# Performance work log

Hardware: AMD Instinct MI355X
Metric: run time of the kernel (lower is better)

The kernel has to match this reference:

```python
import jax, jax.numpy as jnp
import numpy as np

K = 9          # temporal window (kernel_size)
PAD = (K - 1) // 2
BN_EPS = 1e-5


def setup_inputs() -> dict:
    key = jax.random.key(0)
    ks = jax.random.split(key, 9)
    N, Cin, Cout, T, V = 16, 64, 128, 256, 25
    return {
        "x": jax.random.normal(ks[0], (N, Cin, T, V), jnp.float32),
        "conv_w": jax.random.normal(ks[1], (Cout, Cin), jnp.float32) * (1.0 / np.sqrt(Cin)),
        "conv_b": jax.random.normal(ks[2], (Cout,), jnp.float32) * 0.01,
        "gamma": jax.random.uniform(ks[3], (Cout,), jnp.float32, 0.5, 1.5),
        "beta": jax.random.normal(ks[4], (Cout,), jnp.float32) * 0.1,
        "run_mean": jax.random.normal(ks[5], (Cout,), jnp.float32) * 0.1,
        "run_var": jax.random.uniform(ks[6], (Cout,), jnp.float32, 0.5, 1.5),
        "att0": jnp.full((1, Cout, 1, K), 1.0 / K, jnp.float32),
        "A": jax.random.uniform(ks[7], (V, V), jnp.float32),
        "keep_prob": 1,
    }


def reference(x, conv_w, conv_b, gamma, beta, run_mean, run_var, att0, A, keep_prob):
    # 1x1 conv (pointwise channel mix); AvgPool2d((1,1)) is identity for stride=1
    x = jnp.einsum("nctv,oc->notv", x, conv_w) + conv_b[None, :, None, None]
    # BatchNorm2d (eval mode: running stats)
    scale = gamma / jnp.sqrt(run_var + BN_EPS)
    x = x * scale[None, :, None, None] + (beta - run_mean * scale)[None, :, None, None]
    N, C, T, V = x.shape
    # UnfoldTemporalWindows: zero-pad T, gather K temporal shifts -> (N, C, T, K, V)
    xp = jnp.pad(x, ((0, 0), (0, 0), (PAD, PAD), (0, 0)))
    upfold = jnp.stack([xp[:, :, u:u + T, :] for u in range(K)], axis=3)
    # local attention: score each window position against the center frame
    scores = jnp.einsum("nctv,nctuv->nctu", x, upfold) / V
    attn = jax.nn.softmax(scores, axis=-1) + att0
    out = jnp.einsum("nctuv,nctu->nctv", upfold, attn)
    # dropS / dropT are identity at keep_prob == 1 (inference)
    return out
```

## Files before the change

kernel.cpp:

```cpp
#include <hip/hip_runtime.h>
#include <hip/hip_bf16.h>

#define CIN   64
#define COUT  128
#define TT    256
#define VV    25
#define TV    (TT * VV)
#define KW    9
#define PAD   4
#define YROW  28
#define YSTR  (TT * YROW)

typedef __attribute__((ext_vector_type(8))) short short8;
typedef __attribute__((ext_vector_type(4))) float f32x4;

__device__ __forceinline__ unsigned f2b(float f) {
    unsigned u = __builtin_bit_cast(unsigned, f);
    return (u + 0x7FFFu + ((u >> 16) & 1u)) >> 16;
}
__device__ __forceinline__ float lof(unsigned u) {
    return __builtin_bit_cast(float, u << 16);
}
__device__ __forceinline__ float hif(unsigned u) {
    return __builtin_bit_cast(float, u & 0xffff0000u);
}
__device__ __forceinline__ int swz(int row, int cbyte) {
    return row * 128 + ((cbyte & ~15) ^ ((row & 7) << 4)) + (cbyte & 15);
}

__global__ __launch_bounds__(256) void conv_mfma(
    const float* __restrict__ x, const float* __restrict__ w,
    const float* __restrict__ cb, const float* __restrict__ gamma,
    const float* __restrict__ beta, const float* __restrict__ rm,
    const float* __restrict__ rv, unsigned short* __restrict__ y)
{
    __shared__ __align__(16) unsigned short Wl[COUT * 64];
    __shared__ __align__(16) unsigned short Xl[128 * 64];
    __shared__ float sc[COUT];
    __shared__ float of[COUT];

    const int pc  = blockIdx.x;
    const int n   = blockIdx.y;
    const int tid = threadIdx.x;
    const int posbase = pc * 128;

    if (tid < COUT) {
        const float s = gamma[tid] * rsqrtf(rv[tid] + 1e-5f);
        sc[tid] = s;
        of[tid] = cb[tid] * s + beta[tid] - rm[tid] * s;
    }
    for (int idx = tid; idx < 2048; idx += 256) {
        const int c4 = idx & 15, o = idx >> 4;
        const f32x4 wv = *(const f32x4*)(w + o * 64 + c4 * 4);
        uint2 pk;
        pk.x = f2b(wv.x) | (f2b(wv.y) << 16);
        pk.y = f2b(wv.z) | (f2b(wv.w) << 16);
        *(uint2*)((char*)Wl + swz(o, c4 * 8)) = pk;
    }
    for (int idx = tid; idx < 2048; idx += 256) {
        const int pos = idx & 127, c4 = idx >> 7;
        const float* xp = x + (size_t)n * CIN * TV + (size_t)(c4 * 4) * TV + posbase + pos;
        const float a0 = xp[0], a1 = xp[TV], a2 = xp[2 * TV], a3 = xp[3 * TV];
        uint2 pk;
        pk.x = f2b(a0) | (f2b(a1) << 16);
        pk.y = f2b(a2) | (f2b(a3) << 16);
        *(uint2*)((char*)Xl + swz(pos, c4 * 8)) = pk;
    }
    __syncthreads();

    const int wv_ = tid >> 6, lane = tid & 63;
    const int lr = lane & 15, lh = lane >> 4;

    short8 afr[2][2];
#pragma unroll
    for (int m0 = 0; m0 < 2; ++m0)
#pragma unroll
        for (int kh = 0; kh < 2; ++kh)
            afr[m0][kh] = *(const short8*)((const char*)Wl +
                              swz(wv_ * 32 + m0 * 16 + lr, kh * 64 + lh * 16));

    f32x4 acc[2][8];
#pragma unroll
    for (int m0 = 0; m0 < 2; ++m0)
#pragma unroll
        for (int n0 = 0; n0 < 8; ++n0) acc[m0][n0] = (f32x4){0.f, 0.f, 0.f, 0.f};

#pragma unroll
    for (int n0 = 0; n0 < 8; ++n0) {
        const int prow = n0 * 16 + lr;
        const short8 b0 = *(const short8*)((const char*)Xl + swz(prow, lh * 16));
        const short8 b1 = *(const short8*)((const char*)Xl + swz(prow, 64 + lh * 16));
#pragma unroll
        for (int m0 = 0; m0 < 2; ++m0) {
            acc[m0][n0] = __builtin_amdgcn_mfma_f32_16x16x32_bf16(afr[m0][0], b0, acc[m0][n0], 0, 0, 0);
            acc[m0][n0] = __builtin_amdgcn_mfma_f32_16x16x32_bf16(afr[m0][1], b1, acc[m0][n0], 0, 0, 0);
        }
    }

    float scv[2][4], ofv[2][4];
#pragma unroll
    for (int m0 = 0; m0 < 2; ++m0)
#pragma unroll
        for (int r = 0; r < 4; ++r) {
            const int o = wv_ * 32 + m0 * 16 + lh * 4 + r;
            scv[m0][r] = sc[o];
            ofv[m0][r] = of[o];
        }

    const size_t ybase = (size_t)(n * COUT) * YSTR;
#pragma unroll
    for (int m0 = 0; m0 < 2; ++m0)
#pragma unroll
        for (int n0 = 0; n0 < 8; ++n0)
#pragma unroll
            for (int r = 0; r < 4; ++r) {
                const int o = wv_ * 32 + m0 * 16 + lh * 4 + r;
                const int pos = posbase + n0 * 16 + lr;
                const int t = pos / 25;
                const int v = pos - t * 25;
                const float val = acc[m0][n0][r] * scv[m0][r] + ofv[m0][r];
                y[ybase + (size_t)o * YSTR + t * YROW + v] = (unsigned short)f2b(val);
            }
}

#define LOADROW(lr, dst)                                                    \
    {                                                                       \
        const int ub_ = 7 * (lr);                                           \
        const uint2 r0_ = tl2[ub_],     r1_ = tl2[ub_ + 1];                 \
        const uint2 r2_ = tl2[ub_ + 2], r3_ = tl2[ub_ + 3];                 \
        const uint2 r4_ = tl2[ub_ + 4], r5_ = tl2[ub_ + 5];                 \
        const unsigned l_ = tlu[14 * (lr) + 12];                            \
        (dst)[0]  = lof(r0_.x); (dst)[1]  = hif(r0_.x);                     \
        (dst)[2]  = lof(r0_.y); (dst)[3]  = hif(r0_.y);                     \
        (dst)[4]  = lof(r1_.x); (dst)[5]  = hif(r1_.x);                     \
        (dst)[6]  = lof(r1_.y); (dst)[7]  = hif(r1_.y);                     \
        (dst)[8]  = lof(r2_.x); (dst)[9]  = hif(r2_.x);                     \
        (dst)[10] = lof(r2_.y); (dst)[11] = hif(r2_.y);                     \
        (dst)[12] = lof(r3_.x); (dst)[13] = hif(r3_.x);                     \
        (dst)[14] = lof(r3_.y); (dst)[15] = hif(r3_.y);                     \
        (dst)[16] = lof(r4_.x); (dst)[17] = hif(r4_.x);                     \
        (dst)[18] = lof(r4_.y); (dst)[19] = hif(r4_.y);                     \
        (dst)[20] = lof(r5_.x); (dst)[21] = hif(r5_.x);                     \
        (dst)[22] = lof(r5_.y); (dst)[23] = hif(r5_.y);                     \
        (dst)[24] = lof(l_);                                                \
    }

__global__ __launch_bounds__(256) void attn_kernel(
    const unsigned short* __restrict__ y, const float* __restrict__ att0,
    float* __restrict__ out)
{
    __shared__ __align__(16) float sm[TV];
    __shared__ float a0s[KW];

    uint4* tl4 = (uint4*)sm;
    const uint2* tl2 = (const uint2*)sm;
    const unsigned* tlu = (const unsigned*)sm;

    const int nc  = blockIdx.x;
    const int c   = nc & (COUT - 1);
    const int tid = threadIdx.x;

    if (tid < KW) a0s[tid] = att0[c * KW + tid];

    if (tid < 28) {
        const int i = (tid < 14) ? tid : (896 + tid);
        tl4[i] = make_uint4(0, 0, 0, 0);
    }
    const uint4* yg = (const uint4*)(y + (size_t)nc * YSTR);
#pragma unroll
    for (int i = 0; i < 4; ++i) {
        const int ci = tid + i * 256;
        if (ci < 896) tl4[14 + ci] = yg[ci];
    }
    __syncthreads();

    const int t = tid;

    float q[25];
    LOADROW(t + 4, q);

    float osm[25], oa0[25];
    float den;
    {
        float d0 = 0.f, d1 = 0.f;
#pragma unroll
        for (int v = 0; v < 12; ++v)  d0 = fmaf(q[v], q[v], d0);
#pragma unroll
        for (int v = 12; v < 25; ++v) d1 = fmaf(q[v], q[v], d1);
        const float e = __expf((d0 + d1) * (1.f / 25.f));
        den = e;
        const float a = a0s[4];
#pragma unroll
        for (int v = 0; v < 25; ++v) { osm[v] = e * q[v]; oa0[v] = a * q[v]; }
    }

#pragma unroll
    for (int j = 0; j < KW; ++j) {
        if (j == 4) continue;
        float row[25];
        LOADROW(t + j, row);
        float d0 = 0.f, d1 = 0.f;
#pragma unroll
        for (int v = 0; v < 12; ++v)  d0 = fmaf(row[v], q[v], d0);
#pragma unroll
        for (int v = 12; v < 25; ++v) d1 = fmaf(row[v], q[v], d1);
        const float e = __expf((d0 + d1) * (1.f / 25.f));
        den += e;
        const float a = a0s[j];
#pragma unroll
        for (int v = 0; v < 25; ++v) {
            osm[v] = fmaf(e, row[v], osm[v]);
            oa0[v] = fmaf(a, row[v], oa0[v]);
        }
    }

    const float inv = 1.f / den;

    __syncthreads();
    {
        float* dst = &sm[t * 25];
#pragma unroll
        for (int v = 0; v < 25; ++v) dst[v] = fmaf(osm[v], inv, oa0[v]);
    }
    __syncthreads();

    {
        float4* og = (float4*)(out + (size_t)nc * TV);
        const float4* sm4 = (const float4*)sm;
#pragma unroll
        for (int i = 0; i < 7; ++i) {
            const int ci = tid + i * 256;
            if (ci < TV / 4) og[ci] = sm4[ci];
        }
    }
}

extern "C" void kernel_launch(void* const* d_in, const int* in_sizes, int n_in,
                              void* d_out, int out_size, void* d_ws, size_t ws_size,
                              hipStream_t stream)
{
    const float* x     = (const float*)d_in[0];
    const float* w     = (const float*)d_in[1];
    const float* cb    = (const float*)d_in[2];
    const float* gamma = (const float*)d_in[3];
    const float* beta  = (const float*)d_in[4];
    const float* rm    = (const float*)d_in[5];
    const float* rv    = (const float*)d_in[6];
    const float* att0  = (const float*)d_in[7];
    float* out = (float*)d_out;
    unsigned short* y = (unsigned short*)d_ws;

    dim3 gA(TV / 128, 16);
    conv_mfma<<<gA, 256, 0, stream>>>(x, w, cb, gamma, beta, rm, rv, y);

    dim3 gB(16 * COUT);
    attn_kernel<<<gB, 256, 0, stream>>>(y, att0, out);
}
```

Measured before the change: 44.64 us.

## Stage attention rows as fp32 in LDS and use packed FMA math

The attention kernel now unpacks the bf16 intermediate into fp32 once while staging it into shared memory, using a 26-float padded row stride. The per-window dot products and weighted accumulations then run on two-float vectors through inline v_pk_fma_f32. The aim is to drop the repeated bf16-to-fp32 unpacking on every window load and to halve the number of FMA instructions. In exchange, shared memory use roughly doubles, the global load becomes narrower 4-byte accesses with an integer divide per element, and occupancy may fall.

After: 49.79 us. +11.5%, slower.

```diff
diff --git a/kernel.cpp b/kernel.cpp
--- a/kernel.cpp
+++ b/kernel.cpp
@@ -10,9 +10,11 @@
 #define PAD   4
 #define YROW  28
 #define YSTR  (TT * YROW)
+#define RSF   26
 
 typedef __attribute__((ext_vector_type(8))) short short8;
 typedef __attribute__((ext_vector_type(4))) float f32x4;
+typedef __attribute__((ext_vector_type(2))) float f32x2;
 
 __device__ __forceinline__ unsigned f2b(float f) {
     unsigned u = __builtin_bit_cast(unsigned, f);
@@ -23,6 +25,10 @@
 }
 __device__ __forceinline__ float hif(unsigned u) {
     return __builtin_bit_cast(float, u & 0xffff0000u);
+}
+__device__ __forceinline__ f32x2 pkfma(f32x2 a, f32x2 b, f32x2 c) {
+    asm("v_pk_fma_f32 %0, %1, %2, %0" : "+v"(c) : "v"(a), "v"(b));
+    return c;
 }
 __device__ __forceinline__ int swz(int row, int cbyte) {
     return row * 128 + ((cbyte & ~15) ^ ((row & 7) << 4)) + (cbyte & 15);
@@ -123,38 +129,21 @@
             }
 }
 
-#define LOADROW(lr, dst)                                                    \
+#define LOADF(rl, d2, dlast)                                                \
     {                                                                       \
-        const int ub_ = 7 * (lr);                                           \
-        const uint2 r0_ = tl2[ub_],     r1_ = tl2[ub_ + 1];                 \
-        const uint2 r2_ = tl2[ub_ + 2], r3_ = tl2[ub_ + 3];                 \
-        const uint2 r4_ = tl2[ub_ + 4], r5_ = tl2[ub_ + 5];                 \
-        const unsigned l_ = tlu[14 * (lr) + 12];                            \
-        (dst)[0]  = lof(r0_.x); (dst)[1]  = hif(r0_.x);                     \
-        (dst)[2]  = lof(r0_.y); (dst)[3]  = hif(r0_.y);                     \
-        (dst)[4]  = lof(r1_.x); (dst)[5]  = hif(r1_.x);                     \
-        (dst)[6]  = lof(r1_.y); (dst)[7]  = hif(r1_.y);                     \
-        (dst)[8]  = lof(r2_.x); (dst)[9]  = hif(r2_.x);                     \
-        (dst)[10] = lof(r2_.y); (dst)[11] = hif(r2_.y);                     \
-        (dst)[12] = lof(r3_.x); (dst)[13] = hif(r3_.x);                     \
-        (dst)[14] = lof(r3_.y); (dst)[15] = hif(r3_.y);                     \
-        (dst)[16] = lof(r4_.x); (dst)[17] = hif(r4_.x);                     \
-        (dst)[18] = lof(r4_.y); (dst)[19] = hif(r4_.y);                     \
-        (dst)[20] = lof(r5_.x); (dst)[21] = hif(r5_.x);                     \
-        (dst)[22] = lof(r5_.y); (dst)[23] = hif(r5_.y);                     \
-        (dst)[24] = lof(l_);                                                \
+        const f32x2* rp_ = (const f32x2*)(smf + (rl) * RSF);                \
+        d2[0] = rp_[0];  d2[1] = rp_[1];  d2[2] = rp_[2];  d2[3] = rp_[3];  \
+        d2[4] = rp_[4];  d2[5] = rp_[5];  d2[6] = rp_[6];  d2[7] = rp_[7];  \
+        d2[8] = rp_[8];  d2[9] = rp_[9];  d2[10] = rp_[10]; d2[11] = rp_[11];\
+        dlast = smf[(rl) * RSF + 24];                                       \
     }
 
 __global__ __launch_bounds__(256) void attn_kernel(
     const unsigned short* __restrict__ y, const float* __restrict__ att0,
     float* __restrict__ out)
 {
-    __shared__ __align__(16) float sm[TV];
+    __shared__ __align__(16) float smf[264 * RSF];
     __shared__ float a0s[KW];
-
-    uint4* tl4 = (uint4*)sm;
-    const uint2* tl2 = (const uint2*)sm;
-    const unsigned* tlu = (const unsigned*)sm;
 
     const int nc  = blockIdx.x;
     const int c   = nc & (COUT - 1);
@@ -162,71 +151,92 @@
 
     if (tid < KW) a0s[tid] = att0[c * KW + tid];
 
-    if (tid < 28) {
-        const int i = (tid < 14) ? tid : (896 + tid);
-        tl4[i] = make_uint4(0, 0, 0, 0);
-    }
-    const uint4* yg = (const uint4*)(y + (size_t)nc * YSTR);
-#pragma unroll
-    for (int i = 0; i < 4; ++i) {
-        const int ci = tid + i * 256;
-        if (ci < 896) tl4[14 + ci] = yg[ci];
+    if (tid < 104) {
+        smf[tid] = 0.f;
+        smf[260 * RSF + tid] = 0.f;
+    }
+    {
+        const unsigned* ygu = (const unsigned*)(y + (size_t)nc * YSTR);
+#pragma unroll
+        for (int i = 0; i < 14; ++i) {
+            const int idx = tid + i * 256;
+            const unsigned u = ygu[idx];
+            const int t = idx / 14;
+            const int s = (idx - t * 14) * 2;
+            const int dw = (t + 4) * RSF + s;
+            if (s < 24) {
+                *(f32x2*)(smf + dw) = (f32x2){lof(u), hif(u)};
+            } else if (s == 24) {
+                smf[dw] = lof(u);
+            }
+        }
     }
     __syncthreads();
 
     const int t = tid;
 
-    float q[25];
-    LOADROW(t + 4, q);
-
-    float osm[25], oa0[25];
-    float den;
-    {
-        float d0 = 0.f, d1 = 0.f;
-#pragma unroll
-        for (int v = 0; v < 12; ++v)  d0 = fmaf(q[v], q[v], d0);
-#pragma unroll
-        for (int v = 12; v < 25; ++v) d1 = fmaf(q[v], q[v], d1);
-        const float e = __expf((d0 + d1) * (1.f / 25.f));
+    f32x2 q2[12];  float q24;
+    LOADF(t + 4, q2, q24);
+
+    f32x2 osm2[12], oa02[12];
+    float osm24, oa024, den;
+    {
+        f32x2 d2 = (f32x2){0.f, 0.f};
+#pragma unroll
+        for (int k = 0; k < 12; ++k) d2 = pkfma(q2[k], q2[k], d2);
+        const float e = __expf((d2[0] + d2[1] + q24 * q24) * (1.f / 25.f));
         den = e;
         const float a = a0s[4];
-#pragma unroll
-        for (int v = 0; v < 25; ++v) { osm[v] = e * q[v]; oa0[v] = a * q[v]; }
+        const f32x2 ev = (f32x2){e, e}, av = (f32x2){a, a};
+#pragma unroll
+        for (int k = 0; k < 12; ++k) {
+            osm2[k] = pkfma(ev, q2[k], (f32x2){0.f, 0.f});
+            oa02[k] = pkfma(av, q2[k], (f32x2){0.f, 0.f});
+        }
+        osm24 = e * q24;
+        oa024 = a * q24;
     }
 
 #pragma unroll
     for (int j = 0; j < KW; ++j) {
         if (j == 4) continue;
-        float row[25];
-        LOADROW(t + j, row);
-        float d0 = 0.f, d1 = 0.f;
-#pragma unroll
-        for (int v = 0; v < 12; ++v)  d0 = fmaf(row[v], q[v], d0);
-#pragma unroll
-        for (int v = 12; v < 25; ++v) d1 = fmaf(row[v], q[v], d1);
-        const float e = __expf((d0 + d1) * (1.f / 25.f));
+        f32x2 r2[12]; float r24;
+        LOADF(t + j, r2, r24);
+        f32x2 d2 = (f32x2){0.f, 0.f};
+#pragma unroll
+        for (int k = 0; k < 12; ++k) d2 = pkfma(r2[k], q2[k], d2);
+        const float e = __expf((d2[0] + d2[1] + r24 * q24) * (1.f / 25.f));
         den += e;
         const float a = a0s[j];
-#pragma unroll
-        for (int v = 0; v < 25; ++v) {
-            osm[v] = fmaf(e, row[v], osm[v]);
-            oa0[v] = fmaf(a, row[v], oa0[v]);
-        }
+        const f32x2 ev = (f32x2){e, e}, av = (f32x2){a, a};
+#pragma unroll
+        for (int k = 0; k < 12; ++k) {
+            osm2[k] = pkfma(ev, r2[k], osm2[k]);
+            oa02[k] = pkfma(av, r2[k], oa02[k]);
+        }
+        osm24 = fmaf(e, r24, osm24);
+        oa024 = fmaf(a, r24, oa024);
     }
 
     const float inv = 1.f / den;
-
-    __syncthreads();
-    {
-        float* dst = &sm[t * 25];
-#pragma unroll
-        for (int v = 0; v < 25; ++v) dst[v] = fmaf(osm[v], inv, oa0[v]);
+    const f32x2 iv = (f32x2){inv, inv};
+
+    __syncthreads();
+    {
+        float* dst = &smf[t * 25];
+#pragma unroll
+        for (int k = 0; k < 12; ++k) {
+            const f32x2 f = pkfma(iv, osm2[k], oa02[k]);
+            dst[2 * k]     = f[0];
+            dst[2 * k + 1] = f[1];
+        }
+        dst[24] = fmaf(inv, osm24, oa024);
     }
     __syncthreads();
 
     {
         float4* og = (float4*)(out + (size_t)nc * TV);
-        const float4* sm4 = (const float4*)sm;
+        const float4* sm4 = (const float4*)smf;
 #pragma unroll
         for (int i = 0; i < 7; ++i) {
             const int ci = tid + i * 256;
```

## Split each attention row across two threads with shuffle-reduced scores

Applied to the files above, without the earlier changes.

The attention kernel now runs 512 threads per block, and each time step is handled by a pair of lanes that each own half of the 25 joint values. The partial dot products are combined with a cross-lane shuffle before the exponent. This cuts per-thread register use and raises occupancy and latency hiding for the LDS-bound loop. In exchange it adds shuffles, duplicates the exp and softmax work in both lanes, and uses a mask trick for the odd 25th element.

New measurement: 55.32 us. +23.9%, slower.

```diff
diff --git a/kernel.cpp b/kernel.cpp
--- a/kernel.cpp
+++ b/kernel.cpp
@@ -123,29 +123,21 @@
             }
 }
 
-#define LOADROW(lr, dst)                                                    \
+#define LOADHALF(rl, dst)                                                   \
     {                                                                       \
-        const int ub_ = 7 * (lr);                                           \
-        const uint2 r0_ = tl2[ub_],     r1_ = tl2[ub_ + 1];                 \
-        const uint2 r2_ = tl2[ub_ + 2], r3_ = tl2[ub_ + 3];                 \
-        const uint2 r4_ = tl2[ub_ + 4], r5_ = tl2[ub_ + 5];                 \
-        const unsigned l_ = tlu[14 * (lr) + 12];                            \
-        (dst)[0]  = lof(r0_.x); (dst)[1]  = hif(r0_.x);                     \
-        (dst)[2]  = lof(r0_.y); (dst)[3]  = hif(r0_.y);                     \
-        (dst)[4]  = lof(r1_.x); (dst)[5]  = hif(r1_.x);                     \
-        (dst)[6]  = lof(r1_.y); (dst)[7]  = hif(r1_.y);                     \
-        (dst)[8]  = lof(r2_.x); (dst)[9]  = hif(r2_.x);                     \
-        (dst)[10] = lof(r2_.y); (dst)[11] = hif(r2_.y);                     \
-        (dst)[12] = lof(r3_.x); (dst)[13] = hif(r3_.x);                     \
-        (dst)[14] = lof(r3_.y); (dst)[15] = hif(r3_.y);                     \
-        (dst)[16] = lof(r4_.x); (dst)[17] = hif(r4_.x);                     \
-        (dst)[18] = lof(r4_.y); (dst)[19] = hif(r4_.y);                     \
-        (dst)[20] = lof(r5_.x); (dst)[21] = hif(r5_.x);                     \
-        (dst)[22] = lof(r5_.y); (dst)[23] = hif(r5_.y);                     \
-        (dst)[24] = lof(l_);                                                \
-    }
-
-__global__ __launch_bounds__(256) void attn_kernel(
+        const int b2_ = (rl) * 7 + h3;                                      \
+        const uint2 a_ = tl2[b2_], b_ = tl2[b2_ + 1], c_ = tl2[b2_ + 2];    \
+        const unsigned d_ = tlu[14 * (rl) + 12];                            \
+        (dst)[0]  = lof(a_.x); (dst)[1]  = hif(a_.x);                       \
+        (dst)[2]  = lof(a_.y); (dst)[3]  = hif(a_.y);                       \
+        (dst)[4]  = lof(b_.x); (dst)[5]  = hif(b_.x);                       \
+        (dst)[6]  = lof(b_.y); (dst)[7]  = hif(b_.y);                       \
+        (dst)[8]  = lof(c_.x); (dst)[9]  = hif(c_.x);                       \
+        (dst)[10] = lof(c_.y); (dst)[11] = hif(c_.y);                       \
+        (dst)[12] = lof(d_) * hmask;                                        \
+    }
+
+__global__ __launch_bounds__(512) void attn_kernel(
     const unsigned short* __restrict__ y, const float* __restrict__ att0,
     float* __restrict__ out)
 {
@@ -167,50 +159,51 @@
         tl4[i] = make_uint4(0, 0, 0, 0);
     }
     const uint4* yg = (const uint4*)(y + (size_t)nc * YSTR);
-#pragma unroll
-    for (int i = 0; i < 4; ++i) {
-        const int ci = tid + i * 256;
+    {
+        tl4[14 + tid] = yg[tid];
+        const int ci = tid + 512;
         if (ci < 896) tl4[14 + ci] = yg[ci];
     }
     __syncthreads();
 
-    const int t = tid;
-
-    float q[25];
-    LOADROW(t + 4, q);
-
-    float osm[25], oa0[25];
+    const int t  = tid >> 1;
+    const int h  = tid & 1;
+    const int h3 = h * 3;
+    const float hmask = (float)h;
+
+    float q[13];
+    LOADHALF(t + 4, q);
+
+    float osm[13], oa0[13];
     float den;
     {
-        float d0 = 0.f, d1 = 0.f;
-#pragma unroll
-        for (int v = 0; v < 12; ++v)  d0 = fmaf(q[v], q[v], d0);
-#pragma unroll
-        for (int v = 12; v < 25; ++v) d1 = fmaf(q[v], q[v], d1);
-        const float e = __expf((d0 + d1) * (1.f / 25.f));
+        float pd = 0.f;
+#pragma unroll
+        for (int k = 0; k < 13; ++k) pd = fmaf(q[k], q[k], pd);
+        const float full = pd + __shfl_xor(pd, 1);
+        const float e = __expf(full * (1.f / 25.f));
         den = e;
         const float a = a0s[4];
 #pragma unroll
-        for (int v = 0; v < 25; ++v) { osm[v] = e * q[v]; oa0[v] = a * q[v]; }
+        for (int k = 0; k < 13; ++k) { osm[k] = e * q[k]; oa0[k] = a * q[k]; }
     }
 
 #pragma unroll
     for (int j = 0; j < KW; ++j) {
         if (j == 4) continue;
-        float row[25];
-        LOADROW(t + j, row);
-        float d0 = 0.f, d1 = 0.f;
-#pragma unroll
-        for (int v = 0; v < 12; ++v)  d0 = fmaf(row[v], q[v], d0);
-#pragma unroll
-        for (int v = 12; v < 25; ++v) d1 = fmaf(row[v], q[v], d1);
-        const float e = __expf((d0 + d1) * (1.f / 25.f));
+        float row[13];
+        LOADHALF(t + j, row);
+        float pd = 0.f;
+#pragma unroll
+        for (int k = 0; k < 13; ++k) pd = fmaf(row[k], q[k], pd);
+        const float full = pd + __shfl_xor(pd, 1);
+        const float e = __expf(full * (1.f / 25.f));
         den += e;
         const float a = a0s[j];
 #pragma unroll
-        for (int v = 0; v < 25; ++v) {
-            osm[v] = fmaf(e, row[v], osm[v]);
-            oa0[v] = fmaf(a, row[v], oa0[v]);
+        for (int k = 0; k < 13; ++k) {
+            osm[k] = fmaf(e, row[k], osm[k]);
+            oa0[k] = fmaf(a, row[k], oa0[k]);
         }
     }
 
@@ -218,9 +211,10 @@
 
     __syncthreads();
     {
-        float* dst = &sm[t * 25];
-#pragma unroll
-        for (int v = 0; v < 25; ++v) dst[v] = fmaf(osm[v], inv, oa0[v]);
+        float* dst = &sm[t * 25 + h * 12];
+#pragma unroll
+        for (int k = 0; k < 12; ++k) dst[k] = fmaf(osm[k], inv, oa0[k]);
+        if (h) dst[12] = fmaf(osm[12], inv, oa0[12]);
     }
     __syncthreads();
 
@@ -228,8 +222,8 @@
         float4* og = (float4*)(out + (size_t)nc * TV);
         const float4* sm4 = (const float4*)sm;
 #pragma unroll
-        for (int i = 0; i < 7; ++i) {
-            const int ci = tid + i * 256;
+        for (int i = 0; i < 4; ++i) {
+            const int ci = tid + i * 512;
             if (ci < TV / 4) og[ci] = sm4[ci];
         }
     }
@@ -254,5 +248,5 @@
     conv_mfma<<<gA, 256, 0, stream>>>(x, w, cb, gamma, beta, rm, rv, y);
 
     dim3 gB(16 * COUT);
-    attn_kernel<<<gB, 256, 0, stream>>>(y, att0, out);
-}
+    attn_kernel<<<gB, 512, 0, stream>>>(y, att0, out);
+}
```

## Read attention rows directly from global memory with double-buffered prefetch

Applied to the files above, without the earlier changes.

The attention kernel no longer stages the bf16 intermediate tile into shared memory. Each thread now reads its nine window rows straight from global memory (L1/L2 cached), clamping the row index and masking out-of-range rows to zero in place of explicit padding. Loads for the next window row are issued before the current row is unpacked. This removes the shared-memory fill and one barrier, at the cost of redundant global/cache reads (each row is read by up to nine threads), unaligned 8-byte loads, and more registers.

New measurement: 54.01 us. +21.0%, slower.

```diff
diff --git a/kernel.cpp b/kernel.cpp
--- a/kernel.cpp
+++ b/kernel.cpp
@@ -123,26 +123,41 @@
             }
 }
 
-#define LOADROW(lr, dst)                                                    \
+
+#define FETCH(j, b)                                                         \
     {                                                                       \
-        const int ub_ = 7 * (lr);                                           \
-        const uint2 r0_ = tl2[ub_],     r1_ = tl2[ub_ + 1];                 \
-        const uint2 r2_ = tl2[ub_ + 2], r3_ = tl2[ub_ + 3];                 \
-        const uint2 r4_ = tl2[ub_ + 4], r5_ = tl2[ub_ + 5];                 \
-        const unsigned l_ = tlu[14 * (lr) + 12];                            \
-        (dst)[0]  = lof(r0_.x); (dst)[1]  = hif(r0_.x);                     \
-        (dst)[2]  = lof(r0_.y); (dst)[3]  = hif(r0_.y);                     \
-        (dst)[4]  = lof(r1_.x); (dst)[5]  = hif(r1_.x);                     \
-        (dst)[6]  = lof(r1_.y); (dst)[7]  = hif(r1_.y);                     \
-        (dst)[8]  = lof(r2_.x); (dst)[9]  = hif(r2_.x);                     \
-        (dst)[10] = lof(r2_.y); (dst)[11] = hif(r2_.y);                     \
-        (dst)[12] = lof(r3_.x); (dst)[13] = hif(r3_.x);                     \
-        (dst)[14] = lof(r3_.y); (dst)[15] = hif(r3_.y);                     \
-        (dst)[16] = lof(r4_.x); (dst)[17] = hif(r4_.x);                     \
-        (dst)[18] = lof(r4_.y); (dst)[19] = hif(r4_.y);                     \
-        (dst)[20] = lof(r5_.x); (dst)[21] = hif(r5_.x);                     \
-        (dst)[22] = lof(r5_.y); (dst)[23] = hif(r5_.y);                     \
-        (dst)[24] = lof(l_);                                                \
+        const int r_  = t + (j) - PAD;                                      \
+        const int rc_ = min(max(r_, 0), TT - 1);                            \
+        const uint2* rp_ = (const uint2*)(yp + rc_ * YROW);                 \
+        pb0[b] = rp_[0]; pb1[b] = rp_[1]; pb2[b] = rp_[2];                  \
+        pb3[b] = rp_[3]; pb4[b] = rp_[4]; pb5[b] = rp_[5];                  \
+        pb6[b] = ((const unsigned*)rp_)[12];                                \
+        okm[b] = ((unsigned)r_ < (unsigned)TT) ? 0xffffffffu : 0u;          \
+    }
+
+#define UNPACK(b, dst)                                                      \
+    {                                                                       \
+        const unsigned m_ = okm[b];                                         \
+        const unsigned w0_ = pb0[b].x & m_, w1_ = pb0[b].y & m_;            \
+        const unsigned w2_ = pb1[b].x & m_, w3_ = pb1[b].y & m_;            \
+        const unsigned w4_ = pb2[b].x & m_, w5_ = pb2[b].y & m_;            \
+        const unsigned w6_ = pb3[b].x & m_, w7_ = pb3[b].y & m_;            \
+        const unsigned w8_ = pb4[b].x & m_, w9_ = pb4[b].y & m_;            \
+        const unsigned wa_ = pb5[b].x & m_, wb_ = pb5[b].y & m_;            \
+        const unsigned wc_ = pb6[b] & m_;                                   \
+        (dst)[0]  = lof(w0_); (dst)[1]  = hif(w0_);                         \
+        (dst)[2]  = lof(w1_); (dst)[3]  = hif(w1_);                         \
+        (dst)[4]  = lof(w2_); (dst)[5]  = hif(w2_);                         \
+        (dst)[6]  = lof(w3_); (dst)[7]  = hif(w3_);                         \
+        (dst)[8]  = lof(w4_); (dst)[9]  = hif(w4_);                         \
+        (dst)[10] = lof(w5_); (dst)[11] = hif(w5_);                         \
+        (dst)[12] = lof(w6_); (dst)[13] = hif(w6_);                         \
+        (dst)[14] = lof(w7_); (dst)[15] = hif(w7_);                         \
+        (dst)[16] = lof(w8_); (dst)[17] = hif(w8_);                         \
+        (dst)[18] = lof(w9_); (dst)[19] = hif(w9_);                         \
+        (dst)[20] = lof(wa_); (dst)[21] = hif(wa_);                         \
+        (dst)[22] = lof(wb_); (dst)[23] = hif(wb_);                         \
+        (dst)[24] = lof(wc_);                                               \
     }
 
 __global__ __launch_bounds__(256) void attn_kernel(
@@ -150,55 +165,46 @@
     float* __restrict__ out)
 {
     __shared__ __align__(16) float sm[TV];
-    __shared__ float a0s[KW];
-
-    uint4* tl4 = (uint4*)sm;
-    const uint2* tl2 = (const uint2*)sm;
-    const unsigned* tlu = (const unsigned*)sm;
 
     const int nc  = blockIdx.x;
     const int c   = nc & (COUT - 1);
     const int tid = threadIdx.x;
-
-    if (tid < KW) a0s[tid] = att0[c * KW + tid];
-
-    if (tid < 28) {
-        const int i = (tid < 14) ? tid : (896 + tid);
-        tl4[i] = make_uint4(0, 0, 0, 0);
-    }
-    const uint4* yg = (const uint4*)(y + (size_t)nc * YSTR);
-#pragma unroll
-    for (int i = 0; i < 4; ++i) {
-        const int ci = tid + i * 256;
-        if (ci < 896) tl4[14 + ci] = yg[ci];
-    }
-    __syncthreads();
-
-    const int t = tid;
+    const int t   = tid;
+
+    const unsigned short* yp = y + (size_t)nc * YSTR;
+
+    float a0v[KW];
+#pragma unroll
+    for (int j = 0; j < KW; ++j) a0v[j] = att0[c * KW + j];
 
     float q[25];
-    LOADROW(t + 4, q);
+    {
+        const uint2* rp = (const uint2*)(yp + t * YROW);
+        const uint2 a = rp[0], b = rp[1], cc = rp[2], d = rp[3], e = rp[4], f = rp[5];
+        const unsigned g = ((const unsigned*)rp)[12];
+        q[0]  = lof(a.x);  q[1]  = hif(a.x);  q[2]  = lof(a.y);  q[3]  = hif(a.y);
+        q[4]  = lof(b.x);  q[5]  = hif(b.x);  q[6]  = lof(b.y);  q[7]  = hif(b.y);
+        q[8]  = lof(cc.x); q[9]  = hif(cc.x); q[10] = lof(cc.y); q[11] = hif(cc.y);
+        q[12] = lof(d.x);  q[13] = hif(d.x);  q[14] = lof(d.y);  q[15] = hif(d.y);
+        q[16] = lof(e.x);  q[17] = hif(e.x);  q[18] = lof(e.y);  q[19] = hif(e.y);
+        q[20] = lof(f.x);  q[21] = hif(f.x);  q[22] = lof(f.y);  q[23] = hif(f.y);
+        q[24] = lof(g);
+    }
+
+    uint2 pb0[2], pb1[2], pb2[2], pb3[2], pb4[2], pb5[2];
+    unsigned pb6[2], okm[2];
 
     float osm[25], oa0[25];
-    float den;
-    {
-        float d0 = 0.f, d1 = 0.f;
-#pragma unroll
-        for (int v = 0; v < 12; ++v)  d0 = fmaf(q[v], q[v], d0);
-#pragma unroll
-        for (int v = 12; v < 25; ++v) d1 = fmaf(q[v], q[v], d1);
-        const float e = __expf((d0 + d1) * (1.f / 25.f));
-        den = e;
-        const float a = a0s[4];
-#pragma unroll
-        for (int v = 0; v < 25; ++v) { osm[v] = e * q[v]; oa0[v] = a * q[v]; }
-    }
-
+#pragma unroll
+    for (int v = 0; v < 25; ++v) { osm[v] = 0.f; oa0[v] = 0.f; }
+    float den = 0.f;
+
+    FETCH(0, 0);
 #pragma unroll
     for (int j = 0; j < KW; ++j) {
-        if (j == 4) continue;
+        if (j + 1 < KW) FETCH(j + 1, (j + 1) & 1);
         float row[25];
-        LOADROW(t + j, row);
+        UNPACK(j & 1, row);
         float d0 = 0.f, d1 = 0.f;
 #pragma unroll
         for (int v = 0; v < 12; ++v)  d0 = fmaf(row[v], q[v], d0);
@@ -206,7 +212,7 @@
         for (int v = 12; v < 25; ++v) d1 = fmaf(row[v], q[v], d1);
         const float e = __expf((d0 + d1) * (1.f / 25.f));
         den += e;
-        const float a = a0s[j];
+        const float a = a0v[j];
 #pragma unroll
         for (int v = 0; v < 25; ++v) {
             osm[v] = fmaf(e, row[v], osm[v]);
@@ -216,7 +222,6 @@
 
     const float inv = 1.f / den;
 
-    __syncthreads();
     {
         float* dst = &sm[t * 25];
 #pragma unroll
```
